# Kernel tuning notes

Measured on AMD Instinct MI355X. Metric: run time of the kernel, lower is better.

Reference implementation:

```python
import jax, jax.numpy as jnp
import numpy as np

N_BINS = 20


def setup_inputs() -> dict:
    key = jax.random.key(0)
    k1, k2 = jax.random.split(key)
    softmaxes = jax.random.uniform(k1, (1000000, 100), dtype=jnp.float32)
    labels = jax.random.randint(k2, (1000000,), 0, 100, dtype=jnp.int64)
    return {"softmaxes": softmaxes, "labels": labels}


def reference(softmaxes, labels):
    num = softmaxes.shape[0]
    window = num // N_BINS  # equal-frequency bin size

    confidences = jnp.max(softmaxes, axis=1)
    predictions = jnp.argmax(softmaxes, axis=1)
    accuracies = (predictions == labels).astype(softmaxes.dtype)

    order = jnp.argsort(confidences)  # ascending, like torch.sort
    conf_sorted = confidences[order]
    acc_sorted = accuracies[order]

    # only full windows are flushed in the original loop
    n_used = N_BINS * window
    conf_bins = conf_sorted[:n_used].reshape(N_BINS, window)
    acc_bins = acc_sorted[:n_used].reshape(N_BINS, window)

    avg_conf = conf_bins.mean(axis=1)  # [N_BINS]
    avg_acc = acc_bins.mean(axis=1)    # [N_BINS] == ys list

    ece = jnp.sum(jnp.abs(avg_conf - avg_acc)) * (window / num)
    return ece.reshape(1), avg_acc
```

## Files before the change

kernel.cpp:

```cpp
#include <hip/hip_runtime.h>
#include <hip/hip_bf16.h>
#include <math.h>
#include <stdint.h>

#define NROWS 1000000
#define NCOLS 100
#define NBINS 20
#define NB    19
#define W     50000u
#define NH    2049

#define HIST_DW 0u
#define BINS_DW 2052u
#define ZERO_DW 2132u
#define CONF_DW 2136u

__device__ __forceinline__ unsigned int bucket_of(unsigned int bits) {
    if (bits < 0x3F000000u) return 0u;
    unsigned int t = (bits >> 12) - 258048u + 1u;
    return t > 2048u ? 2048u : t;
}

__global__ __launch_bounds__(256) void k1_rowmax(const float* __restrict__ x,
                                                 const int* __restrict__ labels,
                                                 float* __restrict__ conf,
                                                 unsigned int* __restrict__ zero_region) {
    __shared__ float4 ldsx4[1600];
    __shared__ unsigned long long ldsk[64];
    const float* ldsx = (const float*)ldsx4;
    int tid = threadIdx.x;
    int gtid = blockIdx.x * 256 + tid;
    if (gtid < (int)ZERO_DW) zero_region[gtid] = 0u;

    const int NTILES = NROWS / 64;
    for (int tile = blockIdx.x; tile < NTILES; tile += gridDim.x) {
        const float4* src = reinterpret_cast<const float4*>(x) + (size_t)tile * 1600;
        #pragma unroll
        for (int i = 0; i < 7; i++) {
            int v = i * 256 + tid;
            if (v < 1600) ldsx4[v] = src[v];
        }
        if (tid < 64) ldsk[tid] = 0ull;
        __syncthreads();
        int r = tid >> 2, q = tid & 3;
        const float* rowp = ldsx + r * 100 + q * 25;
        float best = rowp[0]; int bi = 0;
        #pragma unroll
        for (int k = 1; k < 25; k++) {
            float vv = rowp[k];
            if (vv > best) { best = vv; bi = k; }
        }
        unsigned long long key =
            ((unsigned long long)__float_as_uint(best) << 32)
            | (unsigned int)(NCOLS - (q * 25 + bi));
        atomicMax(&ldsk[r], key);
        __syncthreads();
        if (tid < 64) {
            unsigned long long kk = ldsk[tid];
            unsigned int bits = (unsigned int)(kk >> 32);
            int idx = NCOLS - (int)(kk & 0xFFFFFFFFu);
            int row = tile * 64 + tid;
            if (idx == labels[row]) bits |= 0x80000000u;
            conf[row] = __uint_as_float(bits);
        }
        __syncthreads();
    }
}

__global__ __launch_bounds__(512) void k2_hist(const float* __restrict__ conf,
                                               unsigned int* __restrict__ hist) {
    __shared__ unsigned int lh[NH];
    for (int i = threadIdx.x; i < NH; i += 512) lh[i] = 0u;
    __syncthreads();
    const uint4* c4 = reinterpret_cast<const uint4*>(conf);
    int stride = gridDim.x * 512;
    for (int i = blockIdx.x * 512 + threadIdx.x; i < NROWS / 4; i += stride) {
        uint4 v = c4[i];
        atomicAdd(&lh[bucket_of(v.x & 0x7FFFFFFFu)], 1u);
        atomicAdd(&lh[bucket_of(v.y & 0x7FFFFFFFu)], 1u);
        atomicAdd(&lh[bucket_of(v.z & 0x7FFFFFFFu)], 1u);
        atomicAdd(&lh[bucket_of(v.w & 0x7FFFFFFFu)], 1u);
    }
    __syncthreads();
    for (int i = threadIdx.x; i < NH; i += 512) {
        unsigned int c = lh[i];
        if (c) atomicAdd(&hist[i], c);
    }
}

__global__ __launch_bounds__(256) void k3_accum(const float* __restrict__ conf,
                                                const unsigned int* __restrict__ hist,
                                                double* __restrict__ bins) {
    __shared__ unsigned int ptab[NH];
    __shared__ unsigned int s[256];
    __shared__ unsigned int bndS[NB];
    __shared__ float sFr[NB];
    __shared__ float sc[4][NBINS], sa[4][NBINS];
    int tid = threadIdx.x;

    unsigned int loc[9];
    unsigned int tot = 0;
    int base = tid * 9;
    #pragma unroll
    for (int k = 0; k < 9; k++) {
        int idx = base + k;
        unsigned int v = (idx < NH) ? hist[idx] : 0u;
        loc[k] = tot; tot += v;
    }
    s[tid] = tot; __syncthreads();
    for (int off = 1; off < 256; off <<= 1) {
        unsigned int v = (tid >= off) ? s[tid - off] : 0u;
        __syncthreads();
        s[tid] += v;
        __syncthreads();
    }
    unsigned int excl = s[tid] - tot;
    #pragma unroll
    for (int k = 0; k < 9; k++) {
        int idx = base + k;
        if (idx < NH) ptab[idx] = excl + loc[k];
    }
    for (int i = tid; i < 4 * NBINS; i += 256) { (&sc[0][0])[i] = 0.f; (&sa[0][0])[i] = 0.f; }
    __syncthreads();

    if (tid < NB) {
        unsigned int r = (unsigned int)(tid + 1) * W;
        int lo = 0, hi = NH - 1;
        while (lo < hi) {
            int mid = (lo + hi + 1) >> 1;
            if (ptab[mid] <= r) lo = mid; else hi = mid - 1;
        }
        unsigned int p = ptab[lo];
        if (p < r) {
            unsigned int cnt = ((lo + 1 < NH) ? ptab[lo + 1] : (unsigned int)NROWS) - p;
            bndS[tid] = (unsigned int)lo;
            sFr[tid]  = (float)(r - p) / (float)cnt;
        } else {
            bndS[tid] = 0xFFFFFFFFu;
        }
    }
    __syncthreads();
    if (tid < NB && bndS[tid] != 0xFFFFFFFFu)
        ptab[bndS[tid]] |= (unsigned int)(tid + 1) << 24;
    __syncthreads();

    int wid = tid >> 6;
    const uint4* c4 = reinterpret_cast<const uint4*>(conf);
    int stride = gridDim.x * 256;
    for (int i = blockIdx.x * 256 + tid; i < NROWS / 4; i += stride) {
        uint4 q = c4[i];
        unsigned int bs[4] = { q.x, q.y, q.z, q.w };
        #pragma unroll
        for (int j = 0; j < 4; j++) {
            unsigned int raw = bs[j];
            float a = (float)(raw >> 31);
            unsigned int bits = raw & 0x7FFFFFFFu;
            float c = __uint_as_float(bits);
            unsigned int e = ptab[bucket_of(bits)];
            unsigned int t = e >> 24;
            if (t == 0u) {
                unsigned int bin = (e & 0xFFFFFFu) / W;
                atomicAdd(&sc[wid][bin], c); atomicAdd(&sa[wid][bin], a);
            } else {
                float fr = sFr[t - 1];
                atomicAdd(&sc[wid][t - 1], c * fr);
                atomicAdd(&sc[wid][t],     c * (1.f - fr));
                atomicAdd(&sa[wid][t - 1], a * fr);
                atomicAdd(&sa[wid][t],     a * (1.f - fr));
            }
        }
    }
    __syncthreads();
    if (tid < NBINS) {
        float tc = sc[0][tid] + sc[1][tid] + sc[2][tid] + sc[3][tid];
        float ta = sa[0][tid] + sa[1][tid] + sa[2][tid] + sa[3][tid];
        atomicAdd(&bins[tid],         (double)tc);
        atomicAdd(&bins[NBINS + tid], (double)ta);
    }
}

__global__ __launch_bounds__(64) void k4_final(const double* __restrict__ bins,
                                               float* __restrict__ out) {
    if (threadIdx.x == 0) {
        double ece = 0.0;
        for (int b = 0; b < NBINS; b++) {
            double avc = bins[b] / (double)W;
            double ava = bins[NBINS + b] / (double)W;
            ece += fabs(avc - ava);
            out[1 + b] = (float)ava;
        }
        out[0] = (float)(ece * ((double)W / (double)NROWS));
    }
}

extern "C" void kernel_launch(void* const* d_in, const int* in_sizes, int n_in,
                              void* d_out, int out_size, void* d_ws, size_t ws_size,
                              hipStream_t stream) {
    const float* x      = (const float*)d_in[0];
    const int*   labels = (const int*)d_in[1];
    float*       out    = (float*)d_out;
    unsigned int* wd    = (unsigned int*)d_ws;

    unsigned int* hist = wd + HIST_DW;
    double*       bins = (double*)(wd + BINS_DW);
    float*        conf = (float*)(wd + CONF_DW);

    k1_rowmax<<<2048, 256, 0, stream>>>(x, labels, conf, wd);
    k2_hist  <<<128, 512, 0, stream>>>(conf, hist);
    k3_accum <<<512, 256, 0, stream>>>(conf, hist, bins);
    k4_final <<<1, 64, 0, stream>>>(bins, out);
}
```

Before: 125.5 us.

## Fuse histogram build into rowmax kernel and add nontemporal loads

Removes the separate histogram kernel: the rowmax kernel now bins each row's confidence as it is produced, using an LDS cache for the high-confidence top buckets and global atomics for the rest. Zeroing of the workspace moves to a small dedicated kernel so the fused kernel's global atomics see a cleared histogram. Input loads switch to nontemporal loads to avoid polluting cache with the streamed 400MB input. This saves one 4MB re-read pass and a launch, but adds global atomic traffic for rows whose buckets fall below the LDS cache range.

```diff
diff --git a/kernel.cpp b/kernel.cpp
--- a/kernel.cpp
+++ b/kernel.cpp
@@ -9,6 +9,9 @@
 #define NB    19
 #define W     50000u
 #define NH    2049
+#define CBASE 1921
+
+typedef float f32x4 __attribute__((ext_vector_type(4)));
 
 #define HIST_DW 0u
 #define BINS_DW 2052u
@@ -21,24 +24,30 @@
     return t > 2048u ? 2048u : t;
 }
 
+__global__ __launch_bounds__(256) void k0_zero(unsigned int* __restrict__ wd) {
+    unsigned int i = blockIdx.x * 256 + threadIdx.x;
+    if (i < ZERO_DW) wd[i] = 0u;
+}
+
 __global__ __launch_bounds__(256) void k1_rowmax(const float* __restrict__ x,
                                                  const int* __restrict__ labels,
                                                  float* __restrict__ conf,
-                                                 unsigned int* __restrict__ zero_region) {
-    __shared__ float4 ldsx4[1600];
+                                                 unsigned int* __restrict__ hist) {
+    __shared__ f32x4 ldsx4[1600];
     __shared__ unsigned long long ldsk[64];
+    __shared__ unsigned int lcache[128];
     const float* ldsx = (const float*)ldsx4;
     int tid = threadIdx.x;
-    int gtid = blockIdx.x * 256 + tid;
-    if (gtid < (int)ZERO_DW) zero_region[gtid] = 0u;
+    if (tid < 128) lcache[tid] = 0u;
 
     const int NTILES = NROWS / 64;
+    const f32x4* xb = reinterpret_cast<const f32x4*>(x);
     for (int tile = blockIdx.x; tile < NTILES; tile += gridDim.x) {
-        const float4* src = reinterpret_cast<const float4*>(x) + (size_t)tile * 1600;
+        const f32x4* src = xb + (size_t)tile * 1600;
         #pragma unroll
         for (int i = 0; i < 7; i++) {
             int v = i * 256 + tid;
-            if (v < 1600) ldsx4[v] = src[v];
+            if (v < 1600) ldsx4[v] = __builtin_nontemporal_load(&src[v]);
         }
         if (tid < 64) ldsk[tid] = 0ull;
         __syncthreads();
@@ -60,31 +69,18 @@
             unsigned int bits = (unsigned int)(kk >> 32);
             int idx = NCOLS - (int)(kk & 0xFFFFFFFFu);
             int row = tile * 64 + tid;
+            unsigned int b = bucket_of(bits);
+            int ci = (int)b - CBASE;
+            if (ci >= 0) atomicAdd(&lcache[ci], 1u);
+            else         atomicAdd(&hist[b], 1u);
             if (idx == labels[row]) bits |= 0x80000000u;
             conf[row] = __uint_as_float(bits);
         }
         __syncthreads();
     }
-}
-
-__global__ __launch_bounds__(512) void k2_hist(const float* __restrict__ conf,
-                                               unsigned int* __restrict__ hist) {
-    __shared__ unsigned int lh[NH];
-    for (int i = threadIdx.x; i < NH; i += 512) lh[i] = 0u;
-    __syncthreads();
-    const uint4* c4 = reinterpret_cast<const uint4*>(conf);
-    int stride = gridDim.x * 512;
-    for (int i = blockIdx.x * 512 + threadIdx.x; i < NROWS / 4; i += stride) {
-        uint4 v = c4[i];
-        atomicAdd(&lh[bucket_of(v.x & 0x7FFFFFFFu)], 1u);
-        atomicAdd(&lh[bucket_of(v.y & 0x7FFFFFFFu)], 1u);
-        atomicAdd(&lh[bucket_of(v.z & 0x7FFFFFFFu)], 1u);
-        atomicAdd(&lh[bucket_of(v.w & 0x7FFFFFFFu)], 1u);
-    }
-    __syncthreads();
-    for (int i = threadIdx.x; i < NH; i += 512) {
-        unsigned int c = lh[i];
-        if (c) atomicAdd(&hist[i], c);
+    if (tid < 128) {
+        unsigned int c = lcache[tid];
+        if (c) atomicAdd(&hist[CBASE + tid], c);
     }
 }
 
@@ -205,8 +201,8 @@
     double*       bins = (double*)(wd + BINS_DW);
     float*        conf = (float*)(wd + CONF_DW);
 
-    k1_rowmax<<<2048, 256, 0, stream>>>(x, labels, conf, wd);
-    k2_hist  <<<128, 512, 0, stream>>>(conf, hist);
+    k0_zero  <<<9, 256, 0, stream>>>(wd);
+    k1_rowmax<<<2048, 256, 0, stream>>>(x, labels, conf, hist);
     k3_accum <<<512, 256, 0, stream>>>(conf, hist, bins);
     k4_final <<<1, 64, 0, stream>>>(bins, out);
 }
```

Measured after the change: 205.9 us. +64.1%, slower.
